# Kernel optimization log

Hardware: AMD Instinct MI355X
Metric: run time of the kernel (lower is better)

Reference implementation:

```python
import jax, jax.numpy as jnp
import numpy as np

N_HEADS = 16

def _rope_tables(seq_len, head_dim, dtype):
    # inv_freq over half the head dim, matching RotaryPositionalEmbedding
    inv_freq = 1.0 / (10000.0 ** (jnp.arange(0, head_dim, 2, dtype=jnp.float32) / head_dim))
    t = jnp.arange(seq_len, dtype=jnp.float32)
    freqs = t[:, None] * inv_freq[None, :]  # [N, d/2]
    # torch code builds cat(freqs,freqs) then slices back to d/2 inside apply_rotary_pos_emb
    return jnp.cos(freqs).astype(dtype), jnp.sin(freqs).astype(dtype)

def _apply_rope(x, cos, sin):
    # x: [B, H, N, d]; cos/sin: [N, d/2] broadcast over B,H
    d = x.shape[-1]
    x1, x2 = x[..., : d // 2], x[..., d // 2 :]
    return jnp.concatenate([x1 * cos - x2 * sin, x1 * sin + x2 * cos], axis=-1)

def setup_inputs() -> dict:
    key = jax.random.key(0)
    k1, k2, k3, k4 = jax.random.split(key, 4)
    B, N, C = 2, 2048, 1024
    x = jax.random.normal(k1, (B, N, C), dtype=jnp.float32)
    w_qkv = jax.random.normal(k2, (C, 3 * C), dtype=jnp.float32) * (C ** -0.5)
    w_proj = jax.random.normal(k3, (C, C), dtype=jnp.float32) * (C ** -0.5)
    b_proj = jax.random.normal(k4, (C,), dtype=jnp.float32) * 0.02
    return {"x": x, "w_qkv": w_qkv, "w_proj": w_proj, "b_proj": b_proj}

def reference(x, w_qkv, w_proj, b_proj):
    B, N, C = x.shape
    H = N_HEADS
    d = C // H
    scale = d ** -0.5
    qkv = (x @ w_qkv).reshape(B, N, 3, H, d)
    qkv = jnp.transpose(qkv, (2, 0, 3, 1, 4))  # [3, B, H, N, d]
    q, k, v = qkv[0], qkv[1], qkv[2]
    cos, sin = _rope_tables(N, d, x.dtype)
    q = _apply_rope(q, cos, sin)
    k = _apply_rope(k, cos, sin)
    attn = jnp.einsum('bhqd,bhkd->bhqk', q, k) * scale  # [B,H,N,N]
    attn = jax.nn.softmax(attn, axis=-1)
    out = jnp.einsum('bhqk,bhkd->bhqd', attn, v)
    out = jnp.transpose(out, (0, 2, 1, 3)).reshape(B, N, C)
    return out @ w_proj + b_proj
```

## Files before the change

kernel.cpp:

```cpp
#include <hip/hip_runtime.h>
#include <math.h>

constexpr int Bc = 2;
constexpr int Nc = 2048;
constexpr int Cc = 1024;
constexpr int Hc = 16;
constexpr int Dc = 64;

typedef __bf16 bf16x8 __attribute__((ext_vector_type(8)));
typedef __bf16 bf16x4 __attribute__((ext_vector_type(4)));
typedef float  f32x4  __attribute__((ext_vector_type(4)));

__device__ __forceinline__ void gload_lds16(const __bf16* g, __bf16* l) {
    __builtin_amdgcn_global_load_lds(
        (const __attribute__((address_space(1))) void*)g,
        (__attribute__((address_space(3))) void*)l, 16, 0, 0);
}

#define MFMA16(A, B, C) __builtin_amdgcn_mfma_f32_16x16x32_bf16(A, B, C, 0, 0, 0)

__global__ void rope_tables(float* __restrict__ cosT, float* __restrict__ sinT) {
    int idx = blockIdx.x * blockDim.x + threadIdx.x;
    if (idx >= Nc * 32) return;
    int n = idx >> 5;
    int j = idx & 31;
    double inv = pow(10000.0, -(double)j / 32.0);
    double ang = (double)n * inv;
    cosT[idx] = (float)cos(ang);
    sinT[idx] = (float)sin(ang);
}

__global__ __launch_bounds__(256) void pack_h(
    const float* __restrict__ src, __bf16* __restrict__ h, int n4) {
    int i = blockIdx.x * 256 + threadIdx.x;
    if (i >= n4) return;
    float4 v = ((const float4*)src)[i];
    bf16x4 hv = {(__bf16)v.x, (__bf16)v.y, (__bf16)v.z, (__bf16)v.w};
    ((bf16x4*)h)[i] = hv;
}

__global__ __launch_bounds__(256) void pack_h_T(
    const float* __restrict__ src, __bf16* __restrict__ h, int K, int Nn) {
    __shared__ float t[64][65];
    const int k0 = blockIdx.y * 64, n0 = blockIdx.x * 64;
    const int c = threadIdx.x & 63, r4 = threadIdx.x >> 6;
    #pragma unroll 4
    for (int p = 0; p < 16; ++p) {
        int kr = p * 4 + r4;
        t[c][kr] = src[(size_t)(k0 + kr) * Nn + n0 + c];
    }
    __syncthreads();
    #pragma unroll 4
    for (int p = 0; p < 16; ++p) {
        int nr = p * 4 + r4;
        h[(size_t)(n0 + nr) * K + k0 + c] = (__bf16)t[nr][c];
    }
}

__global__ __launch_bounds__(256) void pack_hl_T(
    const float* __restrict__ src, __bf16* __restrict__ h,
    __bf16* __restrict__ l, int K, int Nn) {
    __shared__ float t[64][65];
    const int k0 = blockIdx.y * 64, n0 = blockIdx.x * 64;
    const int c = threadIdx.x & 63, r4 = threadIdx.x >> 6;
    #pragma unroll 4
    for (int p = 0; p < 16; ++p) {
        int kr = p * 4 + r4;
        t[c][kr] = src[(size_t)(k0 + kr) * Nn + n0 + c];
    }
    __syncthreads();
    #pragma unroll 4
    for (int p = 0; p < 16; ++p) {
        int nr = p * 4 + r4;
        float v = t[nr][c];
        __bf16 hi = (__bf16)v;
        size_t o = (size_t)(n0 + nr) * K + k0 + c;
        h[o] = hi;
        l[o] = (__bf16)(v - (float)hi);
    }
}

__global__ __launch_bounds__(256) void gemm_qkv_bf(
    const __bf16* __restrict__ Xh, const __bf16* __restrict__ Wh,
    const float* __restrict__ cosT, const float* __restrict__ sinT,
    __bf16* __restrict__ Qh, __bf16* __restrict__ Kh,
    __bf16* __restrict__ Vt) {
    constexpr int K = 1024;
    __shared__ __bf16 sm[18432];

    const int w = threadIdx.x >> 6;
    const int lane = threadIdx.x & 63;
    const int l16 = lane & 15, quad = lane >> 4;
    const int row0 = blockIdx.y * 128;
    const int col0 = blockIdx.x * 128;
    const int wr = (w >> 1) * 64, wc = (w & 1) * 64;
    const int srow = lane & 15, soct = lane >> 4;

    f32x4 acc[4][4];
    #pragma unroll
    for (int mi = 0; mi < 4; ++mi)
        #pragma unroll
        for (int ni = 0; ni < 4; ++ni) acc[mi][ni] = (f32x4){0.f, 0.f, 0.f, 0.f};

    for (int k0 = 0; k0 < K; k0 += 32) {
        __syncthreads();
        #pragma unroll
        for (int i = 0; i < 4; ++i) {
            int c = i * 4 + w;
            int arr = c >> 3, t = c & 7;
            const __bf16* src = (arr == 0)
                ? Xh + (size_t)(row0 + t * 16 + srow) * K
                : Wh + (size_t)(col0 + t * 16 + srow) * K;
            gload_lds16(src + k0 + soct * 8, &sm[arr * 4096 + t * 512]);
        }
        __syncthreads();

        bf16x8 a[4], b[4];
        #pragma unroll
        for (int i = 0; i < 4; ++i) {
            a[i] = *(const bf16x8*)&sm[(wr / 16 + i) * 512 + quad * 128 + l16 * 8];
            b[i] = *(const bf16x8*)&sm[4096 + (wc / 16 + i) * 512 + quad * 128 + l16 * 8];
        }
        #pragma unroll
        for (int mi = 0; mi < 4; ++mi)
            #pragma unroll
            for (int ni = 0; ni < 4; ++ni)
                acc[mi][ni] = MFMA16(a[mi], b[ni], acc[mi][ni]);
    }

    __syncthreads();
    __bf16* T = &sm[w * 4608];

    const int gcol0 = col0 + wc;
    const int region = gcol0 >> 10;
    const int h = (gcol0 & 1023) >> 6;
    const int rb = row0 + wr;
    const int bq = rb >> 11;
    const int nb = rb & 2047;
    const int bh_ = bq * Hc + h;

    if (region < 2) {
        const float scl = (region == 0) ? 0.125f : 1.f;
        #pragma unroll
        for (int mi = 0; mi < 4; ++mi)
            #pragma unroll
            for (int r = 0; r < 4; ++r) {
                int nn = mi * 16 + quad * 4 + r;
                int n = nb + nn;
                float c1 = cosT[n * 32 + l16],      s1 = sinT[n * 32 + l16];
                float c2 = cosT[n * 32 + 16 + l16], s2 = sinT[n * 32 + 16 + l16];
                float x1 = acc[mi][0][r], x2 = acc[mi][2][r];
                float a0 = (x1 * c1 - x2 * s1) * scl;
                float b0 = (x1 * s1 + x2 * c1) * scl;
                x1 = acc[mi][1][r]; x2 = acc[mi][3][r];
                float a1 = (x1 * c2 - x2 * s2) * scl;
                float b1 = (x1 * s2 + x2 * c2) * scl;
                T[nn * 72 + l16]      = (__bf16)a0;
                T[nn * 72 + 16 + l16] = (__bf16)a1;
                T[nn * 72 + 32 + l16] = (__bf16)b0;
                T[nn * 72 + 48 + l16] = (__bf16)b1;
            }
        asm volatile("s_waitcnt lgkmcnt(0)" ::: "memory");
        __bf16* Dst = ((region == 0) ? Qh : Kh) + (size_t)bh_ * Nc * Dc;
        #pragma unroll
        for (int p = 0; p < 8; ++p) {
            int n = p * 8 + (lane >> 3);
            int d8 = (lane & 7) * 8;
            bf16x8 v = *(const bf16x8*)&T[n * 72 + d8];
            *(bf16x8*)(Dst + (size_t)(nb + n) * Dc + d8) = v;
        }
    } else {
        #pragma unroll
        for (int mi = 0; mi < 4; ++mi)
            #pragma unroll
            for (int ni = 0; ni < 4; ++ni)
                #pragma unroll
                for (int r = 0; r < 4; ++r)
                    T[(ni * 16 + l16) * 72 + mi * 16 + quad * 4 + r]
                        = (__bf16)acc[mi][ni][r];
        asm volatile("s_waitcnt lgkmcnt(0)" ::: "memory");
        #pragma unroll
        for (int p = 0; p < 8; ++p) {
            int d = p * 8 + (lane >> 3);
            int n8 = (lane & 7) * 8;
            bf16x8 v = *(const bf16x8*)&T[d * 72 + n8];
            *(bf16x8*)(Vt + ((size_t)bh_ * Dc + d) * Nc + nb + n8) = v;
        }
    }
}

__global__ __launch_bounds__(256) void gemm_proj(
    const __bf16* __restrict__ Ah, const __bf16* __restrict__ Al,
    const __bf16* __restrict__ Bh, const __bf16* __restrict__ Bl,
    const float* __restrict__ bias, float* __restrict__ C,
    int M, int N, int K) {
    __shared__ __bf16 lds[24 * 512];

    const int w = threadIdx.x >> 6;
    const int lane = threadIdx.x & 63;
    const int l16 = lane & 15, quad = lane >> 4;
    const int row0 = blockIdx.y * 64;
    const int col0 = blockIdx.x * 128;
    const int wr = (w >> 1) * 32, wc = (w & 1) * 64;
    const int srow = lane & 15, soct = lane >> 4;

    f32x4 acc[2][4];
    #pragma unroll
    for (int mi = 0; mi < 2; ++mi)
        #pragma unroll
        for (int ni = 0; ni < 4; ++ni) acc[mi][ni] = (f32x4){0.f, 0.f, 0.f, 0.f};

    for (int k0 = 0; k0 < K; k0 += 32) {
        __syncthreads();
        #pragma unroll
        for (int r = 0; r < 6; ++r) {
            int c = r * 4 + w;
            const __bf16* src;
            if (c < 4)       src = Ah + (size_t)(row0 + c * 16 + srow) * K;
            else if (c < 8)  src = Al + (size_t)(row0 + (c - 4) * 16 + srow) * K;
            else if (c < 16) src = Bh + (size_t)(col0 + (c - 8) * 16 + srow) * K;
            else             src = Bl + (size_t)(col0 + (c - 16) * 16 + srow) * K;
            gload_lds16(src + k0 + soct * 8, &lds[c * 512]);
        }
        __syncthreads();

        bf16x8 ah[2], al[2], bh[4], bl[4];
        #pragma unroll
        for (int mi = 0; mi < 2; ++mi) {
            int ia = (wr / 16 + mi) * 512 + quad * 128 + l16 * 8;
            ah[mi] = *(const bf16x8*)&lds[ia];
            al[mi] = *(const bf16x8*)&lds[4 * 512 + ia];
        }
        #pragma unroll
        for (int ni = 0; ni < 4; ++ni) {
            int ib = (wc / 16 + ni) * 512 + quad * 128 + l16 * 8;
            bh[ni] = *(const bf16x8*)&lds[8 * 512 + ib];
            bl[ni] = *(const bf16x8*)&lds[16 * 512 + ib];
        }
        #pragma unroll
        for (int mi = 0; mi < 2; ++mi)
            #pragma unroll
            for (int ni = 0; ni < 4; ++ni) {
                acc[mi][ni] = MFMA16(ah[mi], bl[ni], acc[mi][ni]);
                acc[mi][ni] = MFMA16(al[mi], bh[ni], acc[mi][ni]);
                acc[mi][ni] = MFMA16(ah[mi], bh[ni], acc[mi][ni]);
            }
    }

    #pragma unroll
    for (int mi = 0; mi < 2; ++mi)
        #pragma unroll
        for (int ni = 0; ni < 4; ++ni) {
            int col = col0 + wc + ni * 16 + l16;
            float bv = bias ? bias[col] : 0.f;
            #pragma unroll
            for (int r = 0; r < 4; ++r) {
                int row = row0 + wr + mi * 16 + quad * 4 + r;
                C[(size_t)row * N + col] = acc[mi][ni][r] + bv;
            }
        }
}

__global__ __launch_bounds__(256) void attn_mfma(
    const __bf16* __restrict__ Qh, const __bf16* __restrict__ Kh,
    const __bf16* __restrict__ Vt,
    float* __restrict__ Opart, float* __restrict__ lpart) {
    const int bh = blockIdx.y;
    const int sp = blockIdx.z;
    const int q0 = blockIdx.x * 128;
    const int w = threadIdx.x >> 6;
    const int lane = threadIdx.x & 63;
    const int l16 = lane & 15, quad = lane >> 4;

    const __bf16* Qhb = Qh + (size_t)bh * Nc * Dc;
    const __bf16* Khb = Kh + (size_t)bh * Nc * Dc;
    const __bf16* Vtb = Vt + (size_t)bh * Dc * Nc;

    bf16x8 qh[2][2];
    #pragma unroll
    for (int mi = 0; mi < 2; ++mi)
        #pragma unroll
        for (int ks = 0; ks < 2; ++ks)
            qh[mi][ks] = *(const bf16x8*)(Qhb
                + (size_t)(q0 + w * 32 + mi * 16 + l16) * Dc + ks * 32 + quad * 8);

    f32x4 Oa[2][4];
    #pragma unroll
    for (int mi = 0; mi < 2; ++mi)
        #pragma unroll
        for (int ni = 0; ni < 4; ++ni) Oa[mi][ni] = (f32x4){0.f, 0.f, 0.f, 0.f};
    float lrow[2][4] = {};

    __shared__ __bf16 smT[2][4096];
    __shared__ __bf16 Plds[4][32 * 72];
    __bf16* Pw = Plds[w];

    const int srow = lane & 15;
    const int soct = lane >> 4;

    for (int tile = 0; tile < 16; ++tile) {
        const int kt0 = sp * 1024 + tile * 64;
        __syncthreads();
        #pragma unroll
        for (int i = 0; i < 4; ++i) {
            int c = i * 4 + w;
            int arr = c >> 3, t = c & 7, g = t >> 1, half = t & 1;
            const __bf16* src = (arr == 0)
                ? Khb + (size_t)(kt0 + 16 * g + srow) * Dc + half * 32 + soct * 8
                : Vtb + (size_t)(16 * g + srow) * Nc + kt0 + half * 32 + soct * 8;
            gload_lds16(src, &smT[arr][t * 512]);
        }
        __syncthreads();

        f32x4 S[2][4];
        #pragma unroll
        for (int mi = 0; mi < 2; ++mi)
            #pragma unroll
            for (int kt = 0; kt < 4; ++kt) S[mi][kt] = (f32x4){0.f, 0.f, 0.f, 0.f};

        #pragma unroll
        for (int kt = 0; kt < 4; ++kt) {
            int fb = quad * 128 + l16 * 8;
            bf16x8 kh0 = *(const bf16x8*)&smT[0][(kt * 2 + 0) * 512 + fb];
            bf16x8 kh1 = *(const bf16x8*)&smT[0][(kt * 2 + 1) * 512 + fb];
            #pragma unroll
            for (int mi = 0; mi < 2; ++mi) {
                S[mi][kt] = MFMA16(qh[mi][0], kh0, S[mi][kt]);
                S[mi][kt] = MFMA16(qh[mi][1], kh1, S[mi][kt]);
            }
        }

        #pragma unroll
        for (int mi = 0; mi < 2; ++mi)
            #pragma unroll
            for (int kt = 0; kt < 4; ++kt)
                #pragma unroll
                for (int r = 0; r < 4; ++r) {
                    float p = __expf(S[mi][kt][r]);
                    __bf16 pb = (__bf16)p;
                    Pw[(mi * 16 + quad * 4 + r) * 72 + kt * 16 + l16] = pb;
                    lrow[mi][r] += (float)pb;
                }

        #pragma unroll
        for (int ks2 = 0; ks2 < 2; ++ks2) {
            bf16x8 Pf[2];
            #pragma unroll
            for (int mi = 0; mi < 2; ++mi)
                Pf[mi] = *(const bf16x8*)&Pw[(mi * 16 + l16) * 72 + ks2 * 32 + quad * 8];
            #pragma unroll
            for (int ni = 0; ni < 4; ++ni) {
                bf16x8 vf = *(const bf16x8*)
                    &smT[1][(ni * 2 + ks2) * 512 + quad * 128 + l16 * 8];
                #pragma unroll
                for (int mi = 0; mi < 2; ++mi)
                    Oa[mi][ni] = MFMA16(Pf[mi], vf, Oa[mi][ni]);
            }
        }
    }

    #pragma unroll
    for (int mi = 0; mi < 2; ++mi)
        #pragma unroll
        for (int r = 0; r < 4; ++r) {
            float ps = lrow[mi][r];
            ps += __shfl_xor(ps, 1);
            ps += __shfl_xor(ps, 2);
            ps += __shfl_xor(ps, 4);
            ps += __shfl_xor(ps, 8);
            size_t rowg = (size_t)bh * Nc + q0 + w * 32 + mi * 16 + quad * 4 + r;
            if (l16 == 0) lpart[(size_t)sp * 65536 + rowg] = ps;
            #pragma unroll
            for (int ni = 0; ni < 4; ++ni)
                Opart[((size_t)sp * 65536 + rowg) * Dc + ni * 16 + l16] = Oa[mi][ni][r];
        }
}

__global__ __launch_bounds__(256) void attn_combine(
    const float* __restrict__ Opart, const float* __restrict__ lpart,
    __bf16* __restrict__ Aoh, __bf16* __restrict__ Aol) {
    const int t = blockIdx.x * 256 + threadIdx.x;
    const int row = t >> 4, c4 = t & 15;
    const int bh = row >> 11, n = row & 2047;
    const int b = bh >> 4, h = bh & 15;

    float4 v0 = ((const float4*)(Opart + (size_t)row * Dc))[c4];
    float4 v1 = ((const float4*)(Opart + ((size_t)65536 + row) * Dc))[c4];
    float inv = 1.f / (lpart[row] + lpart[65536 + row]);
    float e[4] = {(v0.x + v1.x) * inv, (v0.y + v1.y) * inv,
                  (v0.z + v1.z) * inv, (v0.w + v1.w) * inv};
    size_t off = ((size_t)(b * Nc + n)) * Cc + h * Dc + c4 * 4;
    bf16x4 hv, lv;
    #pragma unroll
    for (int i = 0; i < 4; ++i) {
        __bf16 hi = (__bf16)e[i];
        hv[i] = hi;
        lv[i] = (__bf16)(e[i] - (float)hi);
    }
    *(bf16x4*)(Aoh + off) = hv;
    *(bf16x4*)(Aol + off) = lv;
}

extern "C" void kernel_launch(void* const* d_in, const int* in_sizes, int n_in,
                              void* d_out, int out_size, void* d_ws, size_t ws_size,
                              hipStream_t stream) {
    const float* x      = (const float*)d_in[0];
    const float* w_qkv  = (const float*)d_in[1];
    const float* w_proj = (const float*)d_in[2];
    const float* b_proj = (const float*)d_in[3];
    float* out = (float*)d_out;

    float* cosT = (float*)d_ws;
    float* sinT = cosT + Nc * 32;
    __bf16* bf = (__bf16*)(sinT + Nc * 32);
    constexpr size_t HS = (size_t)Bc * Hc * Nc * Dc;
    __bf16* Qh  = bf;
    __bf16* Kh  = Qh + HS;
    __bf16* Vt  = Kh + HS;
    __bf16* Xh  = Vt + HS;
    __bf16* Aoh = Xh;
    __bf16* Aol = Xh + HS;
    __bf16* Wqh = Aol + HS;
    __bf16* Wph = Wqh + (size_t)3072 * 1024;
    __bf16* Wpl = Wph + (size_t)1024 * 1024;
    float* Opart = (float*)(Wpl + (size_t)1024 * 1024);
    float* lpart = Opart + (size_t)2 * 65536 * Dc;

    rope_tables<<<(Nc * 32 + 255) / 256, 256, 0, stream>>>(cosT, sinT);
    pack_h<<<(int)(HS / 4 / 256), 256, 0, stream>>>(x, Xh, (int)(HS / 4));
    pack_h_T<<<dim3(3072 / 64, 1024 / 64), 256, 0, stream>>>(
        w_qkv, Wqh, 1024, 3072);
    pack_hl_T<<<dim3(1024 / 64, 1024 / 64), 256, 0, stream>>>(
        w_proj, Wph, Wpl, 1024, 1024);

    gemm_qkv_bf<<<dim3(3072 / 128, 4096 / 128), 256, 0, stream>>>(
        Xh, Wqh, cosT, sinT, Qh, Kh, Vt);

    attn_mfma<<<dim3(Nc / 128, Bc * Hc, 2), 256, 0, stream>>>(
        Qh, Kh, Vt, Opart, lpart);
    attn_combine<<<(65536 * 16) / 256, 256, 0, stream>>>(
        Opart, lpart, Aoh, Aol);

    gemm_proj<<<dim3(1024 / 128, 4096 / 64), 256, 0, stream>>>(
        Aoh, Aol, Wph, Wpl, b_proj, out, 4096, 1024, 1024);
}
```

Before: 251.2 us.

## Fuse prologue kernels, use exp2 with folded scale, compute row sums via MFMA

Merges the four setup kernels (RoPE tables, x cast, w_qkv and w_proj transposes) into one launch that dispatches on block index. This removes three launch gaps. Q is now scaled by log2(e)/sqrt(d) so the softmax can use the hardware exp2 instruction. The per-row probability sum moves from scalar adds plus shuffle reductions to an extra MFMA against a ones vector. That adds matrix work but removes VALU adds and cross-lane reductions.

```diff
diff --git a/kernel.cpp b/kernel.cpp
--- a/kernel.cpp
+++ b/kernel.cpp
@@ -19,64 +19,72 @@
 
 #define MFMA16(A, B, C) __builtin_amdgcn_mfma_f32_16x16x32_bf16(A, B, C, 0, 0, 0)
 
-__global__ void rope_tables(float* __restrict__ cosT, float* __restrict__ sinT) {
-    int idx = blockIdx.x * blockDim.x + threadIdx.x;
-    if (idx >= Nc * 32) return;
-    int n = idx >> 5;
-    int j = idx & 31;
-    double inv = pow(10000.0, -(double)j / 32.0);
-    double ang = (double)n * inv;
-    cosT[idx] = (float)cos(ang);
-    sinT[idx] = (float)sin(ang);
-}
-
-__global__ __launch_bounds__(256) void pack_h(
-    const float* __restrict__ src, __bf16* __restrict__ h, int n4) {
-    int i = blockIdx.x * 256 + threadIdx.x;
-    if (i >= n4) return;
-    float4 v = ((const float4*)src)[i];
-    bf16x4 hv = {(__bf16)v.x, (__bf16)v.y, (__bf16)v.z, (__bf16)v.w};
-    ((bf16x4*)h)[i] = hv;
-}
-
-__global__ __launch_bounds__(256) void pack_h_T(
-    const float* __restrict__ src, __bf16* __restrict__ h, int K, int Nn) {
+#if __has_builtin(__builtin_amdgcn_exp2f)
+#define EXP2F(x) __builtin_amdgcn_exp2f(x)
+#else
+#define EXP2F(x) exp2f(x)
+#endif
+
+#define QSCALE 0.18033688011112042f
+
+__global__ __launch_bounds__(256) void prologue(
+    const float* __restrict__ x, const float* __restrict__ w_qkv,
+    const float* __restrict__ w_proj,
+    float* __restrict__ cosT, float* __restrict__ sinT,
+    __bf16* __restrict__ Xh, __bf16* __restrict__ Wqh,
+    __bf16* __restrict__ Wph, __bf16* __restrict__ Wpl) {
     __shared__ float t[64][65];
-    const int k0 = blockIdx.y * 64, n0 = blockIdx.x * 64;
-    const int c = threadIdx.x & 63, r4 = threadIdx.x >> 6;
-    #pragma unroll 4
-    for (int p = 0; p < 16; ++p) {
-        int kr = p * 4 + r4;
-        t[c][kr] = src[(size_t)(k0 + kr) * Nn + n0 + c];
-    }
-    __syncthreads();
-    #pragma unroll 4
-    for (int p = 0; p < 16; ++p) {
-        int nr = p * 4 + r4;
-        h[(size_t)(n0 + nr) * K + k0 + c] = (__bf16)t[nr][c];
-    }
-}
-
-__global__ __launch_bounds__(256) void pack_hl_T(
-    const float* __restrict__ src, __bf16* __restrict__ h,
-    __bf16* __restrict__ l, int K, int Nn) {
-    __shared__ float t[64][65];
-    const int k0 = blockIdx.y * 64, n0 = blockIdx.x * 64;
-    const int c = threadIdx.x & 63, r4 = threadIdx.x >> 6;
-    #pragma unroll 4
-    for (int p = 0; p < 16; ++p) {
-        int kr = p * 4 + r4;
-        t[c][kr] = src[(size_t)(k0 + kr) * Nn + n0 + c];
-    }
-    __syncthreads();
-    #pragma unroll 4
-    for (int p = 0; p < 16; ++p) {
-        int nr = p * 4 + r4;
-        float v = t[nr][c];
-        __bf16 hi = (__bf16)v;
-        size_t o = (size_t)(n0 + nr) * K + k0 + c;
-        h[o] = hi;
-        l[o] = (__bf16)(v - (float)hi);
+    const int blk = blockIdx.x;
+    const int tid = threadIdx.x;
+
+    if (blk < 256) {
+        int idx = blk * 256 + tid;
+        int n = idx >> 5, j = idx & 31;
+        double inv = pow(10000.0, -(double)j / 32.0);
+        double ang = (double)n * inv;
+        cosT[idx] = (float)cos(ang);
+        sinT[idx] = (float)sin(ang);
+    } else if (blk < 4352) {
+        int i = (blk - 256) * 256 + tid;
+        float4 v = ((const float4*)x)[i];
+        bf16x4 hv = {(__bf16)v.x, (__bf16)v.y, (__bf16)v.z, (__bf16)v.w};
+        ((bf16x4*)Xh)[i] = hv;
+    } else if (blk < 5120) {
+        constexpr int K = 1024, Nn = 3072;
+        int lin = blk - 4352;
+        int n0 = (lin % 48) * 64, k0 = (lin / 48) * 64;
+        int c = tid & 63, r4 = tid >> 6;
+        #pragma unroll 4
+        for (int p = 0; p < 16; ++p) {
+            int kr = p * 4 + r4;
+            t[c][kr] = w_qkv[(size_t)(k0 + kr) * Nn + n0 + c];
+        }
+        __syncthreads();
+        #pragma unroll 4
+        for (int p = 0; p < 16; ++p) {
+            int nr = p * 4 + r4;
+            Wqh[(size_t)(n0 + nr) * K + k0 + c] = (__bf16)t[nr][c];
+        }
+    } else {
+        constexpr int K = 1024, Nn = 1024;
+        int lin = blk - 5120;
+        int n0 = (lin & 15) * 64, k0 = (lin >> 4) * 64;
+        int c = tid & 63, r4 = tid >> 6;
+        #pragma unroll 4
+        for (int p = 0; p < 16; ++p) {
+            int kr = p * 4 + r4;
+            t[c][kr] = w_proj[(size_t)(k0 + kr) * Nn + n0 + c];
+        }
+        __syncthreads();
+        #pragma unroll 4
+        for (int p = 0; p < 16; ++p) {
+            int nr = p * 4 + r4;
+            float v = t[nr][c];
+            __bf16 hi = (__bf16)v;
+            size_t o = (size_t)(n0 + nr) * K + k0 + c;
+            Wph[o] = hi;
+            Wpl[o] = (__bf16)(v - (float)hi);
+        }
     }
 }
 
@@ -140,7 +148,7 @@
     const int bh_ = bq * Hc + h;
 
     if (region < 2) {
-        const float scl = (region == 0) ? 0.125f : 1.f;
+        const float scl = (region == 0) ? QSCALE : 1.f;
         #pragma unroll
         for (int mi = 0; mi < 4; ++mi)
             #pragma unroll
@@ -284,12 +292,16 @@
             qh[mi][ks] = *(const bf16x8*)(Qhb
                 + (size_t)(q0 + w * 32 + mi * 16 + l16) * Dc + ks * 32 + quad * 8);
 
-    f32x4 Oa[2][4];
-    #pragma unroll
-    for (int mi = 0; mi < 2; ++mi)
+    const __bf16 one = (__bf16)1.0f;
+    const bf16x8 onesb = {one, one, one, one, one, one, one, one};
+
+    f32x4 Oa[2][4], Ol[2];
+    #pragma unroll
+    for (int mi = 0; mi < 2; ++mi) {
         #pragma unroll
         for (int ni = 0; ni < 4; ++ni) Oa[mi][ni] = (f32x4){0.f, 0.f, 0.f, 0.f};
-    float lrow[2][4] = {};
+        Ol[mi] = (f32x4){0.f, 0.f, 0.f, 0.f};
+    }
 
     __shared__ __bf16 smT[2][4096];
     __shared__ __bf16 Plds[4][32 * 72];
@@ -336,10 +348,8 @@
             for (int kt = 0; kt < 4; ++kt)
                 #pragma unroll
                 for (int r = 0; r < 4; ++r) {
-                    float p = __expf(S[mi][kt][r]);
-                    __bf16 pb = (__bf16)p;
-                    Pw[(mi * 16 + quad * 4 + r) * 72 + kt * 16 + l16] = pb;
-                    lrow[mi][r] += (float)pb;
+                    float p = EXP2F(S[mi][kt][r]);
+                    Pw[(mi * 16 + quad * 4 + r) * 72 + kt * 16 + l16] = (__bf16)p;
                 }
 
         #pragma unroll
@@ -356,6 +366,9 @@
                 for (int mi = 0; mi < 2; ++mi)
                     Oa[mi][ni] = MFMA16(Pf[mi], vf, Oa[mi][ni]);
             }
+            #pragma unroll
+            for (int mi = 0; mi < 2; ++mi)
+                Ol[mi] = MFMA16(Pf[mi], onesb, Ol[mi]);
         }
     }
 
@@ -363,13 +376,8 @@
     for (int mi = 0; mi < 2; ++mi)
         #pragma unroll
         for (int r = 0; r < 4; ++r) {
-            float ps = lrow[mi][r];
-            ps += __shfl_xor(ps, 1);
-            ps += __shfl_xor(ps, 2);
-            ps += __shfl_xor(ps, 4);
-            ps += __shfl_xor(ps, 8);
             size_t rowg = (size_t)bh * Nc + q0 + w * 32 + mi * 16 + quad * 4 + r;
-            if (l16 == 0) lpart[(size_t)sp * 65536 + rowg] = ps;
+            if (l16 == 0) lpart[(size_t)sp * 65536 + rowg] = Ol[mi][r];
             #pragma unroll
             for (int ni = 0; ni < 4; ++ni)
                 Opart[((size_t)sp * 65536 + rowg) * Dc + ni * 16 + l16] = Oa[mi][ni][r];
@@ -426,12 +434,8 @@
     float* Opart = (float*)(Wpl + (size_t)1024 * 1024);
     float* lpart = Opart + (size_t)2 * 65536 * Dc;
 
-    rope_tables<<<(Nc * 32 + 255) / 256, 256, 0, stream>>>(cosT, sinT);
-    pack_h<<<(int)(HS / 4 / 256), 256, 0, stream>>>(x, Xh, (int)(HS / 4));
-    pack_h_T<<<dim3(3072 / 64, 1024 / 64), 256, 0, stream>>>(
-        w_qkv, Wqh, 1024, 3072);
-    pack_hl_T<<<dim3(1024 / 64, 1024 / 64), 256, 0, stream>>>(
-        w_proj, Wph, Wpl, 1024, 1024);
+    prologue<<<5376, 256, 0, stream>>>(
+        x, w_qkv, w_proj, cosT, sinT, Xh, Wqh, Wph, Wpl);
 
     gemm_qkv_bf<<<dim3(3072 / 128, 4096 / 128), 256, 0, stream>>>(
         Xh, Wqh, cosT, sinT, Qh, Kh, Vt);
```

Result: no change. 251.2 us (+0.0%).
